# Optimization experiments

Measured on AMD Instinct MI355X. Metric: run time of the kernel, lower is better.

## Reference

```python
import jax, jax.numpy as jnp
from jax import lax
import numpy as np

V, D, H = 50257, 128, 256  # vocab, d_model, d_hidden
B, T = 16, 128             # batch, seq_len


def setup_inputs() -> dict:
    key = jax.random.key(0)
    k_ids, k_emb, k_wih, k_whh, k_out = jax.random.split(key, 5)
    s = 0.02
    return {
        "input_ids": jax.random.randint(k_ids, (B, T), 0, V, dtype=jnp.int64 if jax.config.jax_enable_x64 else jnp.int32),
        "embed": jax.random.normal(k_emb, (V, D), jnp.float32) * s,
        "W_ih": jax.random.normal(k_wih, (3 * H, D), jnp.float32) * s,
        "b_ih": jnp.zeros((3 * H,), jnp.float32),
        "W_hh": jax.random.normal(k_whh, (3 * H, H), jnp.float32) * s,
        "b_hh": jnp.zeros((3 * H,), jnp.float32),
        "W_out": jax.random.normal(k_out, (V, H), jnp.float32) * s,
    }


def reference(input_ids, embed, W_ih, b_ih, W_hh, b_hh, W_out):
    # Embedding lookup: [B,T,D]
    x = embed[input_ids]
    # Precompute input-side gate projections for all timesteps: [B,T,3H]
    gx_all = jnp.einsum('btd,gd->btg', x, W_ih) + b_ih

    def step(h, gx):
        # h: [B,H], gx: [B,3H]
        gh = h @ W_hh.T + b_hh  # [B,3H]
        xr, xz, xn = jnp.split(gx, 3, axis=-1)
        hr, hz, hn = jnp.split(gh, 3, axis=-1)
        r = jax.nn.sigmoid(xr + hr)
        z = jax.nn.sigmoid(xz + hz)
        n = jnp.tanh(xn + r * hn)  # PyTorch GRU: r gates the hidden projection
        h_new = (1.0 - z) * n + z * h
        return h_new, h_new

    h0 = jnp.zeros((x.shape[0], W_hh.shape[1]), x.dtype)
    _, hs = lax.scan(step, h0, jnp.swapaxes(gx_all, 0, 1))  # hs: [T,B,H]
    out = jnp.swapaxes(hs, 0, 1)  # [B,T,H]
    # LM head (no bias): [B,T,V]
    return jnp.einsum('bth,vh->btv', out, W_out)
```

## Files before the change

### kernel.cpp

```cpp
#include <hip/hip_runtime.h>
#include <hip/hip_bf16.h>

#define V    50257
#define VPAD 50304
#define DD   128
#define HH   256
#define G3   768
#define BB   16
#define TT   128

typedef _Float16 h2   __attribute__((ext_vector_type(2)));
typedef _Float16 h8   __attribute__((ext_vector_type(8)));
typedef short  bf16x8 __attribute__((ext_vector_type(8)));
typedef float  f32x4  __attribute__((ext_vector_type(4)));

typedef __attribute__((address_space(3))) uint4* lds_u4_t;
typedef const __attribute__((address_space(1))) uint4* gbl_u4_t;

__device__ __forceinline__ void async_copy16(const uint4* g, uint4* lds_base) {
    __builtin_amdgcn_global_load_lds((gbl_u4_t)g, (lds_u4_t)lds_base, 16, 0, 0);
}

#if __has_builtin(__builtin_amdgcn_fdot2)
#define USE_FDOT2 1
#else
#define USE_FDOT2 0
#endif

__device__ __forceinline__ float sigmoid_(float x) { return 1.0f / (1.0f + __expf(-x)); }
__device__ __forceinline__ float tanh_(float x)    { float e = __expf(2.0f * x); return (e - 1.0f) / (e + 1.0f); }

__global__ __launch_bounds__(256) void k_prep(
    const int* __restrict__ ids, const float* __restrict__ embed,
    const float* __restrict__ W_ih, const float* __restrict__ b_ih,
    float* __restrict__ gx,
    const float* __restrict__ Wout, __hip_bfloat16* __restrict__ Wb)
{
    __shared__ float xs[8][DD];
    const int tid = threadIdx.x;

    if (blockIdx.x >= 256) {
        long base = ((long)(blockIdx.x - 256) * 256 + tid) * 8;
        const long VALID = (long)V * HH;
        union { __hip_bfloat16 b[8]; uint4 u; } pk;
        if (base < VALID) {
            float4 f0 = ((const float4*)Wout)[base / 4];
            float4 f1 = ((const float4*)Wout)[base / 4 + 1];
            pk.b[0] = __float2bfloat16(f0.x); pk.b[1] = __float2bfloat16(f0.y);
            pk.b[2] = __float2bfloat16(f0.z); pk.b[3] = __float2bfloat16(f0.w);
            pk.b[4] = __float2bfloat16(f1.x); pk.b[5] = __float2bfloat16(f1.y);
            pk.b[6] = __float2bfloat16(f1.z); pk.b[7] = __float2bfloat16(f1.w);
        } else {
            pk.u = make_uint4(0, 0, 0, 0);
        }
        *(uint4*)(Wb + base) = pk.u;
        return;
    }

    const int row0 = blockIdx.x * 8;

#pragma unroll
    for (int i = 0; i < 4; ++i) {
        int e = tid + i * 256;
        int r = e >> 7, k = e & 127;
        int id = ids[row0 + r];
        xs[r][k] = embed[(long)id * DD + k];
    }
    __syncthreads();

#pragma unroll
    for (int o = 0; o < 3; ++o) {
        int j = tid + o * 256;
        float bias = b_ih[j];
        float acc[8];
#pragma unroll
        for (int r = 0; r < 8; ++r) acc[r] = bias;
        const float4* wrow = (const float4*)(W_ih + (long)j * DD);
        for (int q = 0; q < 32; ++q) {
            float4 w = wrow[q];
#pragma unroll
            for (int r = 0; r < 8; ++r) {
                acc[r] += w.x * xs[r][q * 4 + 0] + w.y * xs[r][q * 4 + 1]
                        + w.z * xs[r][q * 4 + 2] + w.w * xs[r][q * 4 + 3];
            }
        }
#pragma unroll
        for (int r = 0; r < 8; ++r) gx[(long)(row0 + r) * G3 + j] = acc[r];
    }
}

__global__ __launch_bounds__(512)
__attribute__((amdgpu_waves_per_eu(2, 2)))
void k_gru(
    const float* __restrict__ gx, const float* __restrict__ W_hh,
    const float* __restrict__ b_hh, __hip_bfloat16* __restrict__ hout)
{
    __shared__ _Float16 hh[2][HH];
    const int tid = threadIdx.x;
    const int b   = blockIdx.x;
    const int g   = tid >> 1;
    const int u   = tid & 1;

    h2 w[3][64];
#pragma unroll
    for (int o = 0; o < 3; ++o) {
        const float4* wr = (const float4*)(W_hh + (long)(o * 256 + g) * HH + u * 128);
#pragma unroll
        for (int q = 0; q < 32; ++q) {
            float4 f = wr[q];
            w[o][2 * q]     = h2{(_Float16)f.x, (_Float16)f.y};
            w[o][2 * q + 1] = h2{(_Float16)f.z, (_Float16)f.w};
        }
    }
    float bias[3];
#pragma unroll
    for (int o = 0; o < 3; ++o) bias[o] = b_hh[o * 256 + g];

    if (tid < HH) hh[0][tid] = (_Float16)0.0f;
    __syncthreads();

    const float* gxrow = gx + (long)b * TT * G3;
    float cxr = gxrow[g], cxz = gxrow[256 + g], cxn = gxrow[512 + g];
    float hold = 0.0f;

    for (int t = 0; t < TT; ++t) {
        const float* nrow = gxrow + G3;
        float nxr = nrow[g], nxz = nrow[256 + g], nxn = nrow[512 + g];

        float a0a = 0.f, a0b = 0.f, a1a = 0.f, a1b = 0.f, a2a = 0.f, a2b = 0.f;
        const h8* hp8 = ((const h8*)hh[t & 1]) + u * 16;
#pragma unroll
        for (int c = 0; c < 16; ++c) {
            h8 hv = hp8[c];
            const h2* hvp = (const h2*)&hv;
#pragma unroll
            for (int j = 0; j < 4; ++j) {
                h2 hq = hvp[j];
                int p = c * 4 + j;
#if USE_FDOT2
                if (j & 1) {
                    a0b = __builtin_amdgcn_fdot2(w[0][p], hq, a0b, false);
                    a1b = __builtin_amdgcn_fdot2(w[1][p], hq, a1b, false);
                    a2b = __builtin_amdgcn_fdot2(w[2][p], hq, a2b, false);
                } else {
                    a0a = __builtin_amdgcn_fdot2(w[0][p], hq, a0a, false);
                    a1a = __builtin_amdgcn_fdot2(w[1][p], hq, a1a, false);
                    a2a = __builtin_amdgcn_fdot2(w[2][p], hq, a2a, false);
                }
#else
                float hx = (float)hq.x, hy = (float)hq.y;
                if (j & 1) {
                    a0b += (float)w[0][p].x * hx + (float)w[0][p].y * hy;
                    a1b += (float)w[1][p].x * hx + (float)w[1][p].y * hy;
                    a2b += (float)w[2][p].x * hx + (float)w[2][p].y * hy;
                } else {
                    a0a += (float)w[0][p].x * hx + (float)w[0][p].y * hy;
                    a1a += (float)w[1][p].x * hx + (float)w[1][p].y * hy;
                    a2a += (float)w[2][p].x * hx + (float)w[2][p].y * hy;
                }
#endif
            }
        }
        float acc0 = a0a + a0b, acc1 = a1a + a1b, acc2 = a2a + a2b;
        acc0 += __shfl_xor(acc0, 1);
        acc1 += __shfl_xor(acc1, 1);
        acc2 += __shfl_xor(acc2, 1);

        float r = sigmoid_(cxr + acc0 + bias[0]);
        float z = sigmoid_(cxz + acc1 + bias[1]);
        float n = tanh_(cxn + r * (acc2 + bias[2]));
        float hnew = (1.0f - z) * n + z * hold;

        if (u == 0) hh[(t + 1) & 1][g] = (_Float16)hnew;
        else        hout[((long)b * TT + t) * HH + g] = __float2bfloat16(hnew);
        __syncthreads();

        hold = hnew;
        cxr = nxr; cxz = nxz; cxn = nxn;
        gxrow = nrow;
    }
}

__global__ __launch_bounds__(256) void k_head(
    const __hip_bfloat16* __restrict__ Ah, const __hip_bfloat16* __restrict__ Bw,
    float* __restrict__ out)
{
    __shared__ unsigned short As[128 * 64];
    __shared__ unsigned short Bs[128 * 64];
    const int i    = threadIdx.x;
    const int wave = i >> 6, lane = i & 63;
    const int quad = lane >> 4, mr = lane & 15;

    const int lid = blockIdx.x;
    const int xq  = lid & 7;
    const int j   = lid >> 3;
    const int nt  = xq + 8 * (j % 50);
    if (nt >= 393) return;
    const int m0  = (j / 50) * 128;
    const int n0  = nt * 128;

    const int wm0  = (wave >> 1) * 64;
    const int wn0  = (wave & 1) * 64;

    f32x4 acc[4][4];
#pragma unroll
    for (int a = 0; a < 4; ++a)
#pragma unroll
        for (int c = 0; c < 4; ++c) acc[a][c] = (f32x4){0.f, 0.f, 0.f, 0.f};

    const uint4* Ag = (const uint4*)Ah;
    const uint4* Bg = (const uint4*)Bw;
    uint4* Asv = (uint4*)As;
    uint4* Bsv = (uint4*)Bs;

    const uint4* agp[4]; const uint4* bgp[4];
    uint4* alds[4]; uint4* blds[4];
#pragma unroll
    for (int c = 0; c < 4; ++c) {
        int seg   = c * 4 + wave;
        int row   = seg * 8 + (lane >> 3);
        int chunk = (lane & 7) ^ (row & 7);
        agp[c] = Ag + (long)(m0 + row) * 32 + chunk;
        bgp[c] = Bg + (long)(n0 + row) * 32 + chunk;
        alds[c] = Asv + seg * 64;
        blds[c] = Bsv + seg * 64;
    }

    for (int ks = 0; ks < 4; ++ks) {
        __syncthreads();
#pragma unroll
        for (int c = 0; c < 4; ++c) async_copy16(agp[c] + ks * 8, alds[c]);
#pragma unroll
        for (int c = 0; c < 4; ++c) async_copy16(bgp[c] + ks * 8, blds[c]);
        __syncthreads();

#pragma unroll
        for (int kk = 0; kk < 2; ++kk) {
            bf16x8 af[4], bf[4];
#pragma unroll
            for (int wmi = 0; wmi < 4; ++wmi) {
                int row  = wm0 + wmi * 16 + mr;
                int slot = (kk * 4 + quad) ^ (row & 7);
                af[wmi] = *(const bf16x8*)&As[(row * 8 + slot) * 8];
            }
#pragma unroll
            for (int wni = 0; wni < 4; ++wni) {
                int row  = wn0 + wni * 16 + mr;
                int slot = (kk * 4 + quad) ^ (row & 7);
                bf[wni] = *(const bf16x8*)&Bs[(row * 8 + slot) * 8];
            }
#pragma unroll
            for (int wmi = 0; wmi < 4; ++wmi)
#pragma unroll
                for (int wni = 0; wni < 4; ++wni)
                    acc[wmi][wni] = __builtin_amdgcn_mfma_f32_16x16x32_bf16(
                        af[wmi], bf[wni], acc[wmi][wni], 0, 0, 0);
        }
    }

#pragma unroll
    for (int wmi = 0; wmi < 4; ++wmi) {
#pragma unroll
        for (int rr = 0; rr < 4; ++rr) {
            long m = m0 + wm0 + wmi * 16 + quad * 4 + rr;
            float* orow = out + m * (long)V;
#pragma unroll
            for (int wni = 0; wni < 4; ++wni) {
                int n = n0 + wn0 + wni * 16 + mr;
                if (n < V) orow[n] = acc[wmi][wni][rr];
            }
        }
    }
}

extern "C" void kernel_launch(void* const* d_in, const int* in_sizes, int n_in,
                              void* d_out, int out_size, void* d_ws, size_t ws_size,
                              hipStream_t stream) {
    const int*   ids   = (const int*)d_in[0];
    const float* embed = (const float*)d_in[1];
    const float* W_ih  = (const float*)d_in[2];
    const float* b_ih  = (const float*)d_in[3];
    const float* W_hh  = (const float*)d_in[4];
    const float* b_hh  = (const float*)d_in[5];
    const float* W_out = (const float*)d_in[6];
    float* out = (float*)d_out;

    char* ws = (char*)d_ws;
    float*          gx  = (float*)ws;
    __hip_bfloat16* hbf = (__hip_bfloat16*)(ws + 6291456);
    __hip_bfloat16* wbf = (__hip_bfloat16*)(ws + 7340032);

    k_prep<<<6544, 256, 0, stream>>>(ids, embed, W_ih, b_ih, gx, W_out, wbf);
    k_gru<<<16, 512, 0, stream>>>(gx, W_hh, b_hh, hbf);
    k_head<<<6400, 256, 0, stream>>>(hbf, wbf, out);
}
```

Measured before the change: 768.1 us.

## Restructure GRU recurrence to one thread per gate row with LDS gate exchange

The GRU kernel moves from 512 threads, where two threads split each hidden unit's three gate rows and combine via a shuffle, to 768 threads that each own one full W_hh row in registers. Gate pre-activations go to shared memory, and the first 256 threads then apply the nonlinearities and update the hidden state. This removes the cross-lane shuffles and halves the per-thread dot-product chain. In exchange it adds a second barrier per timestep, drops the double-buffered hidden state, and leaves two thirds of the threads idle during the gate update phase.

New measurement: 762.9 us. No clear change (-0.7%).

```diff
diff --git a/kernel.cpp b/kernel.cpp
--- a/kernel.cpp
+++ b/kernel.cpp
@@ -29,6 +29,14 @@
 
 __device__ __forceinline__ float sigmoid_(float x) { return 1.0f / (1.0f + __expf(-x)); }
 __device__ __forceinline__ float tanh_(float x)    { float e = __expf(2.0f * x); return (e - 1.0f) / (e + 1.0f); }
+
+__device__ __forceinline__ float fdot2_(h2 a, h2 b, float c) {
+#if USE_FDOT2
+    return __builtin_amdgcn_fdot2(a, b, c, false);
+#else
+    return c + (float)a.x * (float)b.x + (float)a.y * (float)b.y;
+#endif
+}
 
 __global__ __launch_bounds__(256) void k_prep(
     const int* __restrict__ ids, const float* __restrict__ embed,
@@ -89,95 +97,81 @@
     }
 }
 
-__global__ __launch_bounds__(512)
-__attribute__((amdgpu_waves_per_eu(2, 2)))
+__global__ __launch_bounds__(768)
+__attribute__((amdgpu_waves_per_eu(3, 3)))
 void k_gru(
     const float* __restrict__ gx, const float* __restrict__ W_hh,
     const float* __restrict__ b_hh, __hip_bfloat16* __restrict__ hout)
 {
-    __shared__ _Float16 hh[2][HH];
-    const int tid = threadIdx.x;
-    const int b   = blockIdx.x;
-    const int g   = tid >> 1;
-    const int u   = tid & 1;
-
-    h2 w[3][64];
-#pragma unroll
-    for (int o = 0; o < 3; ++o) {
-        const float4* wr = (const float4*)(W_hh + (long)(o * 256 + g) * HH + u * 128);
-#pragma unroll
-        for (int q = 0; q < 32; ++q) {
-            float4 f = wr[q];
-            w[o][2 * q]     = h2{(_Float16)f.x, (_Float16)f.y};
-            w[o][2 * q + 1] = h2{(_Float16)f.z, (_Float16)f.w};
-        }
-    }
-    float bias[3];
-#pragma unroll
-    for (int o = 0; o < 3; ++o) bias[o] = b_hh[o * 256 + g];
-
-    if (tid < HH) hh[0][tid] = (_Float16)0.0f;
+    __shared__ _Float16 hhs[HH];
+    __shared__ float    ghs[G3];
+
+    const int j = threadIdx.x;
+    const int b = blockIdx.x;
+
+    h2 w[128];
+    const float4* wr = (const float4*)(W_hh + (long)j * HH);
+#pragma unroll
+    for (int qq = 0; qq < 8; ++qq) {
+        float4 f[8];
+#pragma unroll
+        for (int q = 0; q < 8; ++q) f[q] = wr[qq * 8 + q];
+        asm volatile("" ::: "memory");
+#pragma unroll
+        for (int q = 0; q < 8; ++q) {
+            w[qq * 16 + 2 * q]     = h2{(_Float16)f[q].x, (_Float16)f[q].y};
+            w[qq * 16 + 2 * q + 1] = h2{(_Float16)f[q].z, (_Float16)f[q].w};
+        }
+    }
+    const float bias = b_hh[j];
+
+    if (j < HH) hhs[j] = (_Float16)0.0f;
     __syncthreads();
 
-    const float* gxrow = gx + (long)b * TT * G3;
-    float cxr = gxrow[g], cxz = gxrow[256 + g], cxn = gxrow[512 + g];
+    const float* gxb = gx + (long)b * TT * G3;
     float hold = 0.0f;
 
     for (int t = 0; t < TT; ++t) {
-        const float* nrow = gxrow + G3;
-        float nxr = nrow[g], nxz = nrow[256 + g], nxn = nrow[512 + g];
-
-        float a0a = 0.f, a0b = 0.f, a1a = 0.f, a1b = 0.f, a2a = 0.f, a2b = 0.f;
-        const h8* hp8 = ((const h8*)hh[t & 1]) + u * 16;
-#pragma unroll
-        for (int c = 0; c < 16; ++c) {
-            h8 hv = hp8[c];
-            const h2* hvp = (const h2*)&hv;
-#pragma unroll
-            for (int j = 0; j < 4; ++j) {
-                h2 hq = hvp[j];
-                int p = c * 4 + j;
-#if USE_FDOT2
-                if (j & 1) {
-                    a0b = __builtin_amdgcn_fdot2(w[0][p], hq, a0b, false);
-                    a1b = __builtin_amdgcn_fdot2(w[1][p], hq, a1b, false);
-                    a2b = __builtin_amdgcn_fdot2(w[2][p], hq, a2b, false);
-                } else {
-                    a0a = __builtin_amdgcn_fdot2(w[0][p], hq, a0a, false);
-                    a1a = __builtin_amdgcn_fdot2(w[1][p], hq, a1a, false);
-                    a2a = __builtin_amdgcn_fdot2(w[2][p], hq, a2a, false);
+        float xr = 0.f, xz = 0.f, xn = 0.f;
+        if (j < HH) {
+            const float* row = gxb + (long)t * G3;
+            xr = row[j]; xz = row[HH + j]; xn = row[2 * HH + j];
+        }
+
+        float da = 0.f, db = 0.f;
+        const h8* hp8 = (const h8*)hhs;
+#pragma unroll
+        for (int cc = 0; cc < 8; ++cc) {
+            h8 hv0 = hp8[cc * 4 + 0];
+            h8 hv1 = hp8[cc * 4 + 1];
+            h8 hv2 = hp8[cc * 4 + 2];
+            h8 hv3 = hp8[cc * 4 + 3];
+            asm volatile("" ::: "memory");
+            const h8 hvs[4] = {hv0, hv1, hv2, hv3};
+#pragma unroll
+            for (int c2 = 0; c2 < 4; ++c2) {
+                const h2* hp = (const h2*)&hvs[c2];
+#pragma unroll
+                for (int jj = 0; jj < 4; ++jj) {
+                    int p = cc * 16 + c2 * 4 + jj;
+                    if (jj & 1) db = fdot2_(w[p], hp[jj], db);
+                    else        da = fdot2_(w[p], hp[jj], da);
                 }
-#else
-                float hx = (float)hq.x, hy = (float)hq.y;
-                if (j & 1) {
-                    a0b += (float)w[0][p].x * hx + (float)w[0][p].y * hy;
-                    a1b += (float)w[1][p].x * hx + (float)w[1][p].y * hy;
-                    a2b += (float)w[2][p].x * hx + (float)w[2][p].y * hy;
-                } else {
-                    a0a += (float)w[0][p].x * hx + (float)w[0][p].y * hy;
-                    a1a += (float)w[1][p].x * hx + (float)w[1][p].y * hy;
-                    a2a += (float)w[2][p].x * hx + (float)w[2][p].y * hy;
-                }
-#endif
-            }
-        }
-        float acc0 = a0a + a0b, acc1 = a1a + a1b, acc2 = a2a + a2b;
-        acc0 += __shfl_xor(acc0, 1);
-        acc1 += __shfl_xor(acc1, 1);
-        acc2 += __shfl_xor(acc2, 1);
-
-        float r = sigmoid_(cxr + acc0 + bias[0]);
-        float z = sigmoid_(cxz + acc1 + bias[1]);
-        float n = tanh_(cxn + r * (acc2 + bias[2]));
-        float hnew = (1.0f - z) * n + z * hold;
-
-        if (u == 0) hh[(t + 1) & 1][g] = (_Float16)hnew;
-        else        hout[((long)b * TT + t) * HH + g] = __float2bfloat16(hnew);
-        __syncthreads();
-
-        hold = hnew;
-        cxr = nxr; cxz = nxz; cxn = nxn;
-        gxrow = nrow;
+            }
+        }
+        ghs[j] = da + db + bias;
+        __syncthreads();
+
+        if (j < HH) {
+            float r = sigmoid_(xr + ghs[j]);
+            float z = sigmoid_(xz + ghs[HH + j]);
+            float n = tanh_(xn + r * ghs[2 * HH + j]);
+            float hnew = (1.0f - z) * n + z * hold;
+            hold = hnew;
+            hhs[j] = (_Float16)hnew;
+            hout[((long)b * TT + t) * HH + j] = __float2bfloat16(hnew);
+        }
+        __syncthreads();
     }
 }
 
@@ -291,6 +285,6 @@
     __hip_bfloat16* wbf = (__hip_bfloat16*)(ws + 7340032);
 
     k_prep<<<6544, 256, 0, stream>>>(ids, embed, W_ih, b_ih, gx, W_out, wbf);
-    k_gru<<<16, 512, 0, stream>>>(gx, W_hh, b_hh, hbf);
+    k_gru<<<16, 768, 0, stream>>>(gx, W_hh, b_hh, hbf);
     k_head<<<6400, 256, 0, stream>>>(hbf, wbf, out);
 }
```

## Stage GRU input gates via async LDS double buffer and pre-convert W_hh to fp16

Applied to the files above, without the earlier changes.

The GRU kernel now prefetches gx for chunks of 8 timesteps into double-buffered LDS using global_load_lds, instead of issuing per-step global loads. Each step's barrier is replaced with a cheaper lgkmcnt-only barrier. W_hh is converted to fp16 once in the prep kernel, so the GRU prologue loads packed h8 vectors rather than converting fp32 in-kernel. This targets latency on the serial recurrence, which is the critical path, at the cost of extra LDS use and an additional workspace buffer.

After: 731.4 us. -4.8%, faster.

```diff
diff --git a/kernel.cpp b/kernel.cpp
--- a/kernel.cpp
+++ b/kernel.cpp
@@ -30,14 +30,42 @@
 __device__ __forceinline__ float sigmoid_(float x) { return 1.0f / (1.0f + __expf(-x)); }
 __device__ __forceinline__ float tanh_(float x)    { float e = __expf(2.0f * x); return (e - 1.0f) / (e + 1.0f); }
 
+__device__ __forceinline__ float fdot2_(h2 a, h2 b, float c) {
+#if USE_FDOT2
+    return __builtin_amdgcn_fdot2(a, b, c, false);
+#else
+    return c + (float)a.x * (float)b.x + (float)a.y * (float)b.y;
+#endif
+}
+
+#define BARRIER_LDS() do {                                        \
+    asm volatile("s_waitcnt lgkmcnt(0)" ::: "memory");            \
+    __builtin_amdgcn_s_barrier();                                 \
+    __builtin_amdgcn_sched_barrier(0);                            \
+} while (0)
+
 __global__ __launch_bounds__(256) void k_prep(
     const int* __restrict__ ids, const float* __restrict__ embed,
     const float* __restrict__ W_ih, const float* __restrict__ b_ih,
     float* __restrict__ gx,
-    const float* __restrict__ Wout, __hip_bfloat16* __restrict__ Wb)
+    const float* __restrict__ Wout, __hip_bfloat16* __restrict__ Wb,
+    const float* __restrict__ W_hh, _Float16* __restrict__ Wh)
 {
     __shared__ float xs[8][DD];
     const int tid = threadIdx.x;
+
+    if (blockIdx.x >= 6544) {
+        long base = ((long)(blockIdx.x - 6544) * 256 + tid) * 8;
+        float4 f0 = ((const float4*)W_hh)[base / 4];
+        float4 f1 = ((const float4*)W_hh)[base / 4 + 1];
+        union { _Float16 h[8]; uint4 u; } pk;
+        pk.h[0] = (_Float16)f0.x; pk.h[1] = (_Float16)f0.y;
+        pk.h[2] = (_Float16)f0.z; pk.h[3] = (_Float16)f0.w;
+        pk.h[4] = (_Float16)f1.x; pk.h[5] = (_Float16)f1.y;
+        pk.h[6] = (_Float16)f1.z; pk.h[7] = (_Float16)f1.w;
+        *(uint4*)(Wh + base) = pk.u;
+        return;
+    }
 
     if (blockIdx.x >= 256) {
         long base = ((long)(blockIdx.x - 256) * 256 + tid) * 8;
@@ -89,95 +117,104 @@
     }
 }
 
+#define CH   8
+#define NCH  16
+
 __global__ __launch_bounds__(512)
 __attribute__((amdgpu_waves_per_eu(2, 2)))
 void k_gru(
-    const float* __restrict__ gx, const float* __restrict__ W_hh,
+    const float* __restrict__ gx, const _Float16* __restrict__ Wh,
     const float* __restrict__ b_hh, __hip_bfloat16* __restrict__ hout)
 {
+    __shared__ float    gxs[2][CH][G3];
     __shared__ _Float16 hh[2][HH];
+
     const int tid = threadIdx.x;
     const int b   = blockIdx.x;
     const int g   = tid >> 1;
     const int u   = tid & 1;
-
-    h2 w[3][64];
+    const int wv  = tid >> 6;
+    const int ln  = tid & 63;
+
+    h8 w8[3][16];
 #pragma unroll
     for (int o = 0; o < 3; ++o) {
-        const float4* wr = (const float4*)(W_hh + (long)(o * 256 + g) * HH + u * 128);
-#pragma unroll
-        for (int q = 0; q < 32; ++q) {
-            float4 f = wr[q];
-            w[o][2 * q]     = h2{(_Float16)f.x, (_Float16)f.y};
-            w[o][2 * q + 1] = h2{(_Float16)f.z, (_Float16)f.w};
-        }
+        const h8* wrow = (const h8*)(Wh + (long)(o * HH + g) * HH + u * 128);
+#pragma unroll
+        for (int q = 0; q < 16; ++q) w8[o][q] = wrow[q];
     }
     float bias[3];
 #pragma unroll
-    for (int o = 0; o < 3; ++o) bias[o] = b_hh[o * 256 + g];
+    for (int o = 0; o < 3; ++o) bias[o] = b_hh[o * HH + g];
 
     if (tid < HH) hh[0][tid] = (_Float16)0.0f;
-    __syncthreads();
-
-    const float* gxrow = gx + (long)b * TT * G3;
-    float cxr = gxrow[g], cxz = gxrow[256 + g], cxn = gxrow[512 + g];
+
+    const float* gxb = gx + (long)b * TT * G3;
+    auto stage = [&](int c, int buf) {
+        const uint4* src = (const uint4*)(gxb + (long)c * CH * G3);
+        uint4* dstb = (uint4*)(&gxs[buf][0][0]);
+#pragma unroll
+        for (int k = 0; k < 3; ++k)
+            async_copy16(src + (wv * 3 + k) * 64 + ln, dstb + (wv * 3 + k) * 64);
+    };
+
+    stage(0, 0);
     float hold = 0.0f;
 
-    for (int t = 0; t < TT; ++t) {
-        const float* nrow = gxrow + G3;
-        float nxr = nrow[g], nxz = nrow[256 + g], nxn = nrow[512 + g];
-
-        float a0a = 0.f, a0b = 0.f, a1a = 0.f, a1b = 0.f, a2a = 0.f, a2b = 0.f;
-        const h8* hp8 = ((const h8*)hh[t & 1]) + u * 16;
-#pragma unroll
-        for (int c = 0; c < 16; ++c) {
-            h8 hv = hp8[c];
-            const h2* hvp = (const h2*)&hv;
-#pragma unroll
-            for (int j = 0; j < 4; ++j) {
-                h2 hq = hvp[j];
-                int p = c * 4 + j;
-#if USE_FDOT2
-                if (j & 1) {
-                    a0b = __builtin_amdgcn_fdot2(w[0][p], hq, a0b, false);
-                    a1b = __builtin_amdgcn_fdot2(w[1][p], hq, a1b, false);
-                    a2b = __builtin_amdgcn_fdot2(w[2][p], hq, a2b, false);
-                } else {
-                    a0a = __builtin_amdgcn_fdot2(w[0][p], hq, a0a, false);
-                    a1a = __builtin_amdgcn_fdot2(w[1][p], hq, a1a, false);
-                    a2a = __builtin_amdgcn_fdot2(w[2][p], hq, a2a, false);
+    for (int c = 0; c < NCH; ++c) {
+        const int buf = c & 1;
+        if (c + 1 < NCH) {
+            stage(c + 1, buf ^ 1);
+            asm volatile("s_waitcnt vmcnt(3)" ::: "memory");
+        } else {
+            asm volatile("s_waitcnt vmcnt(0)" ::: "memory");
+        }
+        BARRIER_LDS();
+
+        for (int s = 0; s < CH; ++s) {
+            const int t = c * CH + s;
+            float xr = gxs[buf][s][g];
+            float xz = gxs[buf][s][HH + g];
+            float xn = gxs[buf][s][2 * HH + g];
+
+            float a0a = 0.f, a0b = 0.f, a1a = 0.f, a1b = 0.f, a2a = 0.f, a2b = 0.f;
+            const h8* hp8 = ((const h8*)hh[t & 1]) + u * 16;
+#pragma unroll
+            for (int q = 0; q < 16; ++q) {
+                h8 hv = hp8[q];
+                const h2* hq = (const h2*)&hv;
+                const h2* w0 = (const h2*)&w8[0][q];
+                const h2* w1 = (const h2*)&w8[1][q];
+                const h2* w2 = (const h2*)&w8[2][q];
+#pragma unroll
+                for (int jj = 0; jj < 4; ++jj) {
+                    if (jj & 1) {
+                        a0b = fdot2_(w0[jj], hq[jj], a0b);
+                        a1b = fdot2_(w1[jj], hq[jj], a1b);
+                        a2b = fdot2_(w2[jj], hq[jj], a2b);
+                    } else {
+                        a0a = fdot2_(w0[jj], hq[jj], a0a);
+                        a1a = fdot2_(w1[jj], hq[jj], a1a);
+                        a2a = fdot2_(w2[jj], hq[jj], a2a);
+                    }
                 }
-#else
-                float hx = (float)hq.x, hy = (float)hq.y;
-                if (j & 1) {
-                    a0b += (float)w[0][p].x * hx + (float)w[0][p].y * hy;
-                    a1b += (float)w[1][p].x * hx + (float)w[1][p].y * hy;
-                    a2b += (float)w[2][p].x * hx + (float)w[2][p].y * hy;
-                } else {
-                    a0a += (float)w[0][p].x * hx + (float)w[0][p].y * hy;
-                    a1a += (float)w[1][p].x * hx + (float)w[1][p].y * hy;
-                    a2a += (float)w[2][p].x * hx + (float)w[2][p].y * hy;
-                }
-#endif
-            }
-        }
-        float acc0 = a0a + a0b, acc1 = a1a + a1b, acc2 = a2a + a2b;
-        acc0 += __shfl_xor(acc0, 1);
-        acc1 += __shfl_xor(acc1, 1);
-        acc2 += __shfl_xor(acc2, 1);
-
-        float r = sigmoid_(cxr + acc0 + bias[0]);
-        float z = sigmoid_(cxz + acc1 + bias[1]);
-        float n = tanh_(cxn + r * (acc2 + bias[2]));
-        float hnew = (1.0f - z) * n + z * hold;
-
-        if (u == 0) hh[(t + 1) & 1][g] = (_Float16)hnew;
-        else        hout[((long)b * TT + t) * HH + g] = __float2bfloat16(hnew);
-        __syncthreads();
-
-        hold = hnew;
-        cxr = nxr; cxz = nxz; cxn = nxn;
-        gxrow = nrow;
+            }
+            float acc0 = a0a + a0b, acc1 = a1a + a1b, acc2 = a2a + a2b;
+            acc0 += __shfl_xor(acc0, 1);
+            acc1 += __shfl_xor(acc1, 1);
+            acc2 += __shfl_xor(acc2, 1);
+
+            float r = sigmoid_(xr + acc0 + bias[0]);
+            float z = sigmoid_(xz + acc1 + bias[1]);
+            float n = tanh_(xn + r * (acc2 + bias[2]));
+            float hnew = (1.0f - z) * n + z * hold;
+
+            if (u == 0) hh[(t + 1) & 1][g] = (_Float16)hnew;
+            else        hout[((long)b * TT + t) * HH + g] = __float2bfloat16(hnew);
+            BARRIER_LDS();
+
+            hold = hnew;
+        }
     }
 }
 
@@ -286,11 +323,12 @@
     float* out = (float*)d_out;
 
     char* ws = (char*)d_ws;
-    float*          gx  = (float*)ws;
-    __hip_bfloat16* hbf = (__hip_bfloat16*)(ws + 6291456);
-    __hip_bfloat16* wbf = (__hip_bfloat16*)(ws + 7340032);
-
-    k_prep<<<6544, 256, 0, stream>>>(ids, embed, W_ih, b_ih, gx, W_out, wbf);
-    k_gru<<<16, 512, 0, stream>>>(gx, W_hh, b_hh, hbf);
+    float*          gx   = (float*)ws;
+    __hip_bfloat16* hbf  = (__hip_bfloat16*)(ws + 6291456);
+    __hip_bfloat16* wbf  = (__hip_bfloat16*)(ws + 7340032);
+    _Float16*       wh16 = (_Float16*)(ws + 33095680);
+
+    k_prep<<<6640, 256, 0, stream>>>(ids, embed, W_ih, b_ih, gx, W_out, wbf, W_hh, wh16);
+    k_gru<<<16, 512, 0, stream>>>(gx, wh16, b_hh, hbf);
     k_head<<<6400, 256, 0, stream>>>(hbf, wbf, out);
 }
```
